# Optimization experiments

Measured on AMD Instinct MI355X. Metric: run time of the kernel, lower is better.

Reference implementation:

```python
import jax, jax.numpy as jnp
import numpy as np

N = 50000      # nodes
E = 800000     # edges (before self-loops)
NFEAT = 128
NHID = 32
H = 8
NCLASS = 47
NEG_SLOPE = 0.2  # PyG GATv2Conv default


def gatv2_layer(x, src, dst, Wl, Wr, att, b, n):
    """One GATv2Conv layer (concat over heads). att: [H, C]."""
    h, c = att.shape
    xl = (x @ Wl).reshape(n, h, c)  # source transform (lin_l)
    xr = (x @ Wr).reshape(n, h, c)  # target transform (lin_r)
    e = jax.nn.leaky_relu(xl[src] + xr[dst], NEG_SLOPE)   # [E, H, C]
    logits = jnp.einsum('ehc,hc->eh', e, att)             # [E, H]
    # segment softmax over incoming edges of each target node
    m = jax.ops.segment_max(logits, dst, num_segments=n)  # [N, H]
    alpha = jnp.exp(logits - m[dst])
    denom = jax.ops.segment_sum(alpha, dst, num_segments=n)
    alpha = alpha / (denom[dst] + 1e-16)
    msg = xl[src] * alpha[:, :, None]                     # [E, H, C]
    out = jax.ops.segment_sum(msg, dst, num_segments=n)   # [N, H, C]
    return out.reshape(n, h * c) + b


def setup_inputs():
    key = jax.random.key(0)
    ks = jax.random.split(key, 16)
    s = 0.1
    x = jax.random.normal(ks[0], (N, NFEAT), jnp.float32)
    edge_index = jax.random.randint(ks[1], (2, E), 0, N)
    HID = H * NHID  # 256
    params = dict(
        Wl0=jax.random.normal(ks[2], (NFEAT, HID), jnp.float32) * s,
        Wr0=jax.random.normal(ks[3], (NFEAT, HID), jnp.float32) * s,
        a0=jax.random.normal(ks[4], (H, NHID), jnp.float32) * s,
        b0=jnp.zeros((HID,), jnp.float32),
        Wl1=jax.random.normal(ks[5], (HID, HID), jnp.float32) * s,
        Wr1=jax.random.normal(ks[6], (HID, HID), jnp.float32) * s,
        a1=jax.random.normal(ks[7], (H, NHID), jnp.float32) * s,
        b1=jnp.zeros((HID,), jnp.float32),
        Wl2=jax.random.normal(ks[8], (HID, NCLASS), jnp.float32) * s,
        Wr2=jax.random.normal(ks[9], (HID, NCLASS), jnp.float32) * s,
        a2=jax.random.normal(ks[10], (1, NCLASS), jnp.float32) * s,
        b2=jnp.zeros((NCLASS,), jnp.float32),
    )
    return {"x": x, "edge_index": edge_index, **params}


def reference(x, edge_index, Wl0, Wr0, a0, b0, Wl1, Wr1, a1, b1, Wl2, Wr2, a2, b2):
    n = x.shape[0]
    # PyG GATv2Conv adds self-loops by default
    loops = jnp.arange(n, dtype=edge_index.dtype)
    src = jnp.concatenate([edge_index[0], loops])
    dst = jnp.concatenate([edge_index[1], loops])
    h = gatv2_layer(x, src, dst, Wl0, Wr0, a0, b0, n)
    h = jax.nn.elu(h)
    h = gatv2_layer(h, src, dst, Wl1, Wr1, a1, b1, n)
    h = jax.nn.elu(h)
    h = gatv2_layer(h, src, dst, Wl2, Wr2, a2, b2, n)
    return jax.nn.log_softmax(h, axis=-1)
```

## Files before the change

kernel.cpp:

```cpp
#include <hip/hip_runtime.h>
#include <cmath>


#define NFEAT 128
#define HID 256
#define NCLS 47
#define L2PAD 64
#define LOG2E 1.44269504088896340736f

typedef __attribute__((ext_vector_type(8))) short bf16x8;
typedef __attribute__((ext_vector_type(4))) float f32x4;
typedef __attribute__((ext_vector_type(2))) float f32x2;

__device__ __forceinline__ unsigned short f2b(float f) {
  unsigned int u = __builtin_bit_cast(unsigned int, f);
  u += 0x7FFFu + ((u >> 16) & 1u);
  return (unsigned short)(u >> 16);
}
__device__ __forceinline__ float b2f(unsigned short s) {
  return __builtin_bit_cast(float, (unsigned int)s << 16);
}
__device__ __forceinline__ f32x2 b2f2(unsigned int u) {
  return (f32x2){__builtin_bit_cast(float, u << 16),
                 __builtin_bit_cast(float, u & 0xFFFF0000u)};
}
__device__ __forceinline__ void glds16(const unsigned short* g, unsigned short* l) {
  __builtin_amdgcn_global_load_lds(
      (const __attribute__((address_space(1))) unsigned int*)g,
      (__attribute__((address_space(3))) unsigned int*)l, 16, 0, 0);
}

__global__ void k_cast_bf16(const float* __restrict__ in,
                            unsigned short* __restrict__ out, int n4,
                            int* __restrict__ deg, int n) {
  int i = blockIdx.x * blockDim.x + threadIdx.x;
  if (i < n4) {
    float4 v = reinterpret_cast<const float4*>(in)[i];
    ushort4 o = {f2b(v.x), f2b(v.y), f2b(v.z), f2b(v.w)};
    reinterpret_cast<ushort4*>(out)[i] = o;
  } else {
    int j = i - n4;
    if (j < n) deg[j] = 1;
  }
}

struct WtArgs {
  const float* W[6];
  unsigned short* WT[6];
  int K[6], M[6], off[6], total;
  const float* att;
  float* att48;
};
__global__ void k_wt_all(WtArgs a) {
  int i = blockIdx.x * blockDim.x + threadIdx.x;
  if (i >= a.total) {
    int j = i - a.total;
    if (j < 48) a.att48[j] = (j < NCLS) ? a.att[j] * LOG2E : 0.f;
    return;
  }
  int s = 0;
  #pragma unroll
  for (int j = 1; j < 6; ++j) if (i >= a.off[j]) s = j;
  int jj = i - a.off[s];
  int K = a.K[s], M = a.M[s];
  int m = jj / K, k = jj - m * K;
  a.WT[s][jj] = (m < M) ? f2b(a.W[s][(size_t)k * M + m]) : (unsigned short)0;
}

__global__ void k_count(const int* __restrict__ dst, int* __restrict__ deg, int e) {
  int i = blockIdx.x * blockDim.x + threadIdx.x;
  if (i < e) atomicAdd(&deg[dst[i]], 1);
}

__global__ __launch_bounds__(256) void k_bsum(const int* __restrict__ deg,
                                              int* __restrict__ bsum, int n) {
  int t = threadIdx.x;
  int base = blockIdx.x * 1024 + t * 4;
  int s = 0;
  if (base + 3 < n) {
    int4 v = *reinterpret_cast<const int4*>(deg + base);
    s = v.x + v.y + v.z + v.w;
  } else {
    for (int j = 0; j < 4; ++j) { int i = base + j; if (i < n) s += deg[i]; }
  }
  #pragma unroll
  for (int off = 1; off < 64; off <<= 1) s += __shfl_xor(s, off, 64);
  __shared__ int wsum[4];
  if ((t & 63) == 0) wsum[t >> 6] = s;
  __syncthreads();
  if (t == 0) bsum[blockIdx.x] = wsum[0] + wsum[1] + wsum[2] + wsum[3];
}

__global__ void k_scanb(int* __restrict__ bsum, int nb) {
  int lane = threadIdx.x;
  int v = (lane < nb) ? bsum[lane] : 0;
  #pragma unroll
  for (int off = 1; off < 64; off <<= 1) {
    int u = __shfl_up(v, off, 64);
    if (lane >= off) v += u;
  }
  if (lane < nb) bsum[lane] = v;
}

__global__ __launch_bounds__(256) void k_scanfinal(const int* __restrict__ deg,
                                                   const int* __restrict__ bscan,
                                                   int* __restrict__ rowptr,
                                                   int* __restrict__ adj,
                                                   int* __restrict__ vdst,
                                                   int* __restrict__ cursor, int n) {
  int t = threadIdx.x, b = blockIdx.x;
  int base = b * 1024 + t * 4;
  int v0 = 0, v1 = 0, v2 = 0, v3 = 0;
  if (base + 3 < n) {
    int4 v = *reinterpret_cast<const int4*>(deg + base);
    v0 = v.x; v1 = v.y; v2 = v.z; v3 = v.w;
  } else {
    if (base < n) v0 = deg[base];
    if (base + 1 < n) v1 = deg[base + 1];
    if (base + 2 < n) v2 = deg[base + 2];
    if (base + 3 < n) v3 = deg[base + 3];
  }
  int s = v0 + v1 + v2 + v3;
  int incl = s;
  #pragma unroll
  for (int off = 1; off < 64; off <<= 1) {
    int u = __shfl_up(incl, off, 64);
    if ((t & 63) >= off) incl += u;
  }
  __shared__ int wsum[4];
  int w = t >> 6, l = t & 63;
  if (l == 63) wsum[w] = incl;
  __syncthreads();
  int woff = 0;
  for (int j = 0; j < w; ++j) woff += wsum[j];
  int excl = incl - s + woff;
  int boff = (b == 0) ? 0 : bscan[b - 1];
  int p0 = boff + excl;
  int p1 = p0 + v0, p2 = p1 + v1, p3 = p2 + v2, p4 = p3 + v3;
  if (base < n)     { rowptr[base + 1] = p1; adj[p0] = base;     vdst[p0] = base;     cursor[base]     = p0 + 1; }
  if (base + 1 < n) { rowptr[base + 2] = p2; adj[p1] = base + 1; vdst[p1] = base + 1; cursor[base + 1] = p1 + 1; }
  if (base + 2 < n) { rowptr[base + 3] = p3; adj[p2] = base + 2; vdst[p2] = base + 2; cursor[base + 2] = p2 + 1; }
  if (base + 3 < n) { rowptr[base + 4] = p4; adj[p3] = base + 3; vdst[p3] = base + 3; cursor[base + 3] = p3 + 1; }
  if (b == 0 && t == 0) rowptr[0] = 0;
}

__global__ void k_scatter(const int* __restrict__ src, const int* __restrict__ dst,
                          int* __restrict__ cursor, int* __restrict__ adj,
                          int* __restrict__ vdst, int e) {
  int i = blockIdx.x * blockDim.x + threadIdx.x;
  if (i < e) {
    int d = dst[i];
    int p = atomicAdd(&cursor[d], 1);
    adj[p] = src[i];
    vdst[p] = d;
  }
}

__global__ __launch_bounds__(512) void gemm_dual_bf16_128(
    const unsigned short* __restrict__ X, const unsigned short* __restrict__ WlT,
    const unsigned short* __restrict__ WrT, unsigned short* __restrict__ XL,
    unsigned short* __restrict__ XR, int N, int K, int Mpad) {
  __shared__ __align__(16) unsigned short S[3 * 128 * 64];
  unsigned short* Xs = S;
  unsigned short* Ls = S + 8192;
  unsigned short* Rs = S + 16384;

  const int t = threadIdx.x;
  const int col0 = blockIdx.x * 128;
  const int row0 = blockIdx.y * 128;
  const int w = t >> 6, lane = t & 63;
  const int wr = w >> 2, wc = w & 3;
  const int r15 = lane & 15, kc = lane >> 4;
  const bool tail = (row0 + 128 > N);

  const int row_a = t >> 3,          c16_a = t & 7;
  const int row_b = (t + 512) >> 3,  c16_b = t & 7;
  const int sg_a = (c16_a ^ (row_a & 7)) * 8;
  const int sg_b = (c16_b ^ (row_b & 7)) * 8;
  unsigned short* d0 = S + w * 512;
  unsigned short* d1 = S + 4096 + w * 512;

  f32x4 accL[4][2], accR[4][2];
  #pragma unroll
  for (int rf = 0; rf < 4; ++rf)
    #pragma unroll
    for (int cf = 0; cf < 2; ++cf) {
      accL[rf][cf] = (f32x4){0.f, 0.f, 0.f, 0.f};
      accR[rf][cf] = (f32x4){0.f, 0.f, 0.f, 0.f};
    }

  for (int k0 = 0; k0 < K; k0 += 64) {
    glds16(WlT + (size_t)(col0 + row_a) * K + k0 + sg_a, d0 + 8192);
    glds16(WlT + (size_t)(col0 + row_b) * K + k0 + sg_b, d1 + 8192);
    glds16(WrT + (size_t)(col0 + row_a) * K + k0 + sg_a, d0 + 16384);
    glds16(WrT + (size_t)(col0 + row_b) * K + k0 + sg_b, d1 + 16384);
    if (!tail) {
      glds16(X + (size_t)(row0 + row_a) * K + k0 + sg_a, d0);
      glds16(X + (size_t)(row0 + row_b) * K + k0 + sg_b, d1);
    } else {
      uint4 va = (uint4){0, 0, 0, 0}, vb = (uint4){0, 0, 0, 0};
      if (row0 + row_a < N)
        va = *reinterpret_cast<const uint4*>(X + (size_t)(row0 + row_a) * K + k0 + sg_a);
      if (row0 + row_b < N)
        vb = *reinterpret_cast<const uint4*>(X + (size_t)(row0 + row_b) * K + k0 + sg_b);
      *reinterpret_cast<uint4*>(Xs + row_a * 64 + c16_a * 8) = va;
      *reinterpret_cast<uint4*>(Xs + row_b * 64 + c16_b * 8) = vb;
    }
    __syncthreads();

    #pragma unroll
    for (int ks = 0; ks < 2; ++ks) {
      const int c16 = ks * 4 + kc;
      bf16x8 a[4];
      #pragma unroll
      for (int rf = 0; rf < 4; ++rf) {
        const int rA = wr * 64 + rf * 16 + r15;
        a[rf] = *reinterpret_cast<const bf16x8*>(Xs + rA * 64 + ((c16 ^ (rA & 7)) * 8));
      }
      #pragma unroll
      for (int cf = 0; cf < 2; ++cf) {
        const int rB = wc * 32 + cf * 16 + r15;
        const int so = rB * 64 + ((c16 ^ (rB & 7)) * 8);
        const bf16x8 bl = *reinterpret_cast<const bf16x8*>(Ls + so);
        const bf16x8 br = *reinterpret_cast<const bf16x8*>(Rs + so);
        #pragma unroll
        for (int rf = 0; rf < 4; ++rf) {
          accL[rf][cf] = __builtin_amdgcn_mfma_f32_16x16x32_bf16(a[rf], bl, accL[rf][cf], 0, 0, 0);
          accR[rf][cf] = __builtin_amdgcn_mfma_f32_16x16x32_bf16(a[rf], br, accR[rf][cf], 0, 0, 0);
        }
      }
    }
    __syncthreads();
  }

  #pragma unroll
  for (int rf = 0; rf < 4; ++rf) {
    #pragma unroll
    for (int cf = 0; cf < 2; ++cf) {
      int cc = col0 + wc * 32 + cf * 16 + r15;
      #pragma unroll
      for (int i = 0; i < 4; ++i) {
        int rr = row0 + wr * 64 + rf * 16 + kc * 4 + i;
        if (rr < N) {
          XL[(size_t)rr * Mpad + cc] = f2b(accL[rf][cf][i]);
          XR[(size_t)rr * Mpad + cc] = f2b(accR[rf][cf][i]);
        }
      }
    }
  }
}

__global__ __launch_bounds__(256) void gemm_dual_bf16(
    const unsigned short* __restrict__ X, const unsigned short* __restrict__ WlT,
    const unsigned short* __restrict__ WrT, unsigned short* __restrict__ XL,
    unsigned short* __restrict__ XR, int N, int K, int Mpad) {
  __shared__ __align__(16) unsigned short S[3 * 64 * 64];
  unsigned short* Xs = S;
  unsigned short* Ls = S + 4096;
  unsigned short* Rs = S + 8192;

  const int t = threadIdx.x;
  const int col0 = blockIdx.x * 64;
  const int row0 = blockIdx.y * 64;
  const int w = t >> 6, lane = t & 63;
  const int r15 = lane & 15, kc = lane >> 4;
  const bool tail = (row0 + 64 > N);

  const int rowa = t >> 3, c16a = t & 7;
  const int rowb = (t + 256) >> 3, c16b = t & 7;
  const int sga = (c16a ^ (rowa & 7)) * 8;
  const int sgb = (c16b ^ (rowb & 7)) * 8;
  unsigned short* ldst0 = S + (w * 512);
  unsigned short* ldst1 = S + (2048 + w * 512);

  f32x4 accL[4], accR[4];
  #pragma unroll
  for (int i = 0; i < 4; ++i) {
    accL[i] = (f32x4){0.f, 0.f, 0.f, 0.f};
    accR[i] = (f32x4){0.f, 0.f, 0.f, 0.f};
  }

  const int rA = 16 * w + r15;

  for (int k0 = 0; k0 < K; k0 += 64) {
    glds16(WlT + (size_t)(col0 + rowa) * K + k0 + sga, ldst0 + 4096);
    glds16(WlT + (size_t)(col0 + rowb) * K + k0 + sgb, ldst1 + 4096);
    glds16(WrT + (size_t)(col0 + rowa) * K + k0 + sga, ldst0 + 8192);
    glds16(WrT + (size_t)(col0 + rowb) * K + k0 + sgb, ldst1 + 8192);
    if (!tail) {
      glds16(X + (size_t)(row0 + rowa) * K + k0 + sga, ldst0);
      glds16(X + (size_t)(row0 + rowb) * K + k0 + sgb, ldst1);
    } else {
      uint4 va = (uint4){0, 0, 0, 0}, vb = (uint4){0, 0, 0, 0};
      if (row0 + rowa < N)
        va = *reinterpret_cast<const uint4*>(X + (size_t)(row0 + rowa) * K + k0 + sga);
      if (row0 + rowb < N)
        vb = *reinterpret_cast<const uint4*>(X + (size_t)(row0 + rowb) * K + k0 + sgb);
      *reinterpret_cast<uint4*>(Xs + rowa * 64 + c16a * 8) = va;
      *reinterpret_cast<uint4*>(Xs + rowb * 64 + c16b * 8) = vb;
    }
    __syncthreads();

    #pragma unroll
    for (int ks = 0; ks < 2; ++ks) {
      const int c16 = ks * 4 + kc;
      const bf16x8 a = *reinterpret_cast<const bf16x8*>(
          Xs + rA * 64 + ((c16 ^ (rA & 7)) * 8));
      #pragma unroll
      for (int nf = 0; nf < 4; ++nf) {
        const int rB = nf * 16 + r15;
        const int so = rB * 64 + ((c16 ^ (rB & 7)) * 8);
        const bf16x8 bl = *reinterpret_cast<const bf16x8*>(Ls + so);
        const bf16x8 br = *reinterpret_cast<const bf16x8*>(Rs + so);
        accL[nf] = __builtin_amdgcn_mfma_f32_16x16x32_bf16(a, bl, accL[nf], 0, 0, 0);
        accR[nf] = __builtin_amdgcn_mfma_f32_16x16x32_bf16(a, br, accR[nf], 0, 0, 0);
      }
    }
    __syncthreads();
  }

  #pragma unroll
  for (int nf = 0; nf < 4; ++nf) {
    int cc = col0 + nf * 16 + r15;
    #pragma unroll
    for (int i = 0; i < 4; ++i) {
      int rr = row0 + 16 * w + kc * 4 + i;
      if (rr < N) {
        XL[(size_t)rr * Mpad + cc] = f2b(accL[nf][i]);
        XR[(size_t)rr * Mpad + cc] = f2b(accR[nf][i]);
      }
    }
  }
}

__global__ __launch_bounds__(1024) void gat_node_hc(
    const unsigned short* __restrict__ xl, const unsigned short* __restrict__ xr,
    const float* __restrict__ att, const float* __restrict__ bias,
    const int* __restrict__ rowptr, const int* __restrict__ adj,
    unsigned short* __restrict__ out, int n) {
  int wid = (blockIdx.x * blockDim.x + threadIdx.x) >> 6;
  int lane = threadIdx.x & 63;
  if (wid >= n) return;
  const int q = lane & 31, half = lane >> 5;

  const uint4 xrp = *reinterpret_cast<const uint4*>(xr + (size_t)wid * HID + q * 8);
  const f32x2 xr2[4] = {b2f2(xrp.x), b2f2(xrp.y), b2f2(xrp.z), b2f2(xrp.w)};
  const float4 af0 = *reinterpret_cast<const float4*>(att + q * 8);
  const float4 af1 = *reinterpret_cast<const float4*>(att + q * 8 + 4);
  const f32x2 a2[4] = {{af0.x, af0.y}, {af0.z, af0.w},
                       {af1.x, af1.y}, {af1.z, af1.w}};

  float m = -1e30f, denom = 0.f;
  f32x2 acc[4] = {{0.f, 0.f}, {0.f, 0.f}, {0.f, 0.f}, {0.f, 0.f}};

  const int beg = rowptr[wid], end = rowptr[wid + 1];
  int i = beg + half;
  bool act = i < end;
  int u = adj[act ? i : beg];
  uint4 p = *reinterpret_cast<const uint4*>(xl + (size_t)u * HID + q * 8);

  for (int base = beg; base < end; base += 2) {
    const int i2 = base + 2 + half;
    const bool act2 = i2 < end;
    const int u2 = adj[act2 ? i2 : beg];
    const uint4 p2 = *reinterpret_cast<const uint4*>(xl + (size_t)u2 * HID + q * 8);

    const f32x2 x2[4] = {b2f2(p.x), b2f2(p.y), b2f2(p.z), b2f2(p.w)};
    f32x2 s2 = {0.f, 0.f};
    #pragma unroll
    for (int j = 0; j < 4; ++j) {
      f32x2 z = x2[j] + xr2[j];
      f32x2 lz = 0.2f * z;
      f32x2 r = {fmaxf(z.x, lz.x), fmaxf(z.y, lz.y)};
      s2 += r * a2[j];
    }
    float part = s2.x + s2.y;
    part += __shfl_xor(part, 1, 64);
    part += __shfl_xor(part, 2, 64);
    if (!act) part = -1e30f;
    if (__any(part > m + 8.f)) {
      float mn = fmaxf(m, part);
      float so = __expf(m - mn);
      float wn = act ? __expf(part - mn) : 0.f;
      denom = denom * so + wn;
      #pragma unroll
      for (int j = 0; j < 4; ++j) acc[j] = acc[j] * so + wn * x2[j];
      m = mn;
    } else {
      float wn = act ? __expf(part - m) : 0.f;
      denom += wn;
      #pragma unroll
      for (int j = 0; j < 4; ++j) acc[j] += wn * x2[j];
    }
    p = p2;
    act = act2;
  }

  float mo = __shfl_xor(m, 32, 64);
  float ms = fmaxf(m, mo);
  float sc = __expf(m - ms);
  denom *= sc;
  denom += __shfl_xor(denom, 32, 64);
  #pragma unroll
  for (int j = 0; j < 4; ++j) {
    acc[j] *= sc;
    acc[j].x += __shfl_xor(acc[j].x, 32, 64);
    acc[j].y += __shfl_xor(acc[j].y, 32, 64);
  }

  if (half == 0) {
    const float inv = 1.f / (denom + 1e-16f);
    const float4 bf0 = *reinterpret_cast<const float4*>(bias + q * 8);
    const float4 bf1 = *reinterpret_cast<const float4*>(bias + q * 8 + 4);
    float o[8] = {acc[0].x * inv + bf0.x, acc[0].y * inv + bf0.y,
                  acc[1].x * inv + bf0.z, acc[1].y * inv + bf0.w,
                  acc[2].x * inv + bf1.x, acc[2].y * inv + bf1.y,
                  acc[3].x * inv + bf1.z, acc[3].y * inv + bf1.w};
    #pragma unroll
    for (int j = 0; j < 8; ++j) o[j] = o[j] > 0.f ? o[j] : (__expf(o[j]) - 1.f);
    uint4 ov;
    ov.x = (unsigned)f2b(o[0]) | ((unsigned)f2b(o[1]) << 16);
    ov.y = (unsigned)f2b(o[2]) | ((unsigned)f2b(o[3]) << 16);
    ov.z = (unsigned)f2b(o[4]) | ((unsigned)f2b(o[5]) << 16);
    ov.w = (unsigned)f2b(o[6]) | ((unsigned)f2b(o[7]) << 16);
    *reinterpret_cast<uint4*>(out + (size_t)wid * HID + q * 8) = ov;
  }
}

__global__ __launch_bounds__(256) void k_logit_l2(
    const unsigned short* __restrict__ xl, const unsigned short* __restrict__ xr,
    const float* __restrict__ att48, const int* __restrict__ adj,
    const int* __restrict__ vdst, float* __restrict__ logit, int total) {
  int i = blockIdx.x * blockDim.x + threadIdx.x;
  if (i >= total) return;
  const int u = adj[i], v = vdst[i];
  const uint4* pu = reinterpret_cast<const uint4*>(xl + (size_t)u * L2PAD);
  const uint4* pv = reinterpret_cast<const uint4*>(xr + (size_t)v * L2PAD);
  f32x2 s2 = {0.f, 0.f};
  #pragma unroll
  for (int b = 0; b < 6; ++b) {
    const uint4 xu = pu[b], xv = pv[b];
    const f32x2* a2 = reinterpret_cast<const f32x2*>(att48 + b * 8);
    const unsigned ua[4] = {xu.x, xu.y, xu.z, xu.w};
    const unsigned va[4] = {xv.x, xv.y, xv.z, xv.w};
    #pragma unroll
    for (int j = 0; j < 4; ++j) {
      f32x2 z = b2f2(ua[j]) + b2f2(va[j]);
      f32x2 lz = 0.2f * z;
      f32x2 r = {fmaxf(z.x, lz.x), fmaxf(z.y, lz.y)};
      s2 += r * a2[j];
    }
  }
  logit[i] = s2.x + s2.y;
}

__global__ __launch_bounds__(1024) void gat_node_l2(
    const unsigned short* __restrict__ xl, const float* __restrict__ logit,
    const float* __restrict__ bias, const int* __restrict__ rowptr,
    const int* __restrict__ adj, float* __restrict__ out, int n) {
  int wid = (blockIdx.x * blockDim.x + threadIdx.x) >> 6;
  int lane = threadIdx.x & 63;
  if (wid >= n) return;
  const bool act = lane < NCLS;
  const int beg = rowptr[wid], end = rowptr[wid + 1];

  float mx = -1e30f;
  for (int i = beg + lane; i < end; i += 64) mx = fmaxf(mx, logit[i]);
  #pragma unroll
  for (int off = 1; off < 64; off <<= 1) mx = fmaxf(mx, __shfl_xor(mx, off, 64));

  float denom = 0.f, acc = 0.f;
  int i = beg;
  for (; i + 1 < end; i += 2) {
    int u0 = adj[i], u1 = adj[i + 1];
    float w0 = exp2f(logit[i] - mx);
    float w1 = exp2f(logit[i + 1] - mx);
    float x0 = act ? b2f(xl[(size_t)u0 * L2PAD + lane]) : 0.f;
    float x1 = act ? b2f(xl[(size_t)u1 * L2PAD + lane]) : 0.f;
    denom += w0 + w1;
    acc += w0 * x0 + w1 * x1;
  }
  if (i < end) {
    int u0 = adj[i];
    float w0 = exp2f(logit[i] - mx);
    float x0 = act ? b2f(xl[(size_t)u0 * L2PAD + lane]) : 0.f;
    denom += w0;
    acc += w0 * x0;
  }

  float r = acc / (denom + 1e-16f) + (act ? bias[lane] : 0.f);
  float rm = act ? r : -1e30f;
  #pragma unroll
  for (int off = 1; off < 64; off <<= 1) rm = fmaxf(rm, __shfl_xor(rm, off, 64));
  float se = act ? __expf(r - rm) : 0.f;
  #pragma unroll
  for (int off = 1; off < 64; off <<= 1) se += __shfl_xor(se, off, 64);
  if (act) out[(size_t)wid * NCLS + lane] = r - rm - __logf(se);
}

extern "C" void kernel_launch(void* const* d_in, const int* in_sizes, int n_in,
                              void* d_out, int out_size, void* d_ws, size_t ws_size,
                              hipStream_t stream) {
  const float* x   = (const float*)d_in[0];
  const int* ei    = (const int*)d_in[1];
  const float* Wl0 = (const float*)d_in[2];
  const float* Wr0 = (const float*)d_in[3];
  const float* a0  = (const float*)d_in[4];
  const float* b0  = (const float*)d_in[5];
  const float* Wl1 = (const float*)d_in[6];
  const float* Wr1 = (const float*)d_in[7];
  const float* a1  = (const float*)d_in[8];
  const float* b1  = (const float*)d_in[9];
  const float* Wl2 = (const float*)d_in[10];
  const float* Wr2 = (const float*)d_in[11];
  const float* a2  = (const float*)d_in[12];
  const float* b2  = (const float*)d_in[13];

  const int N = in_sizes[0] / NFEAT;
  const int E = in_sizes[1] / 2;
  const int* src = ei;
  const int* dst = ei + E;
  const int total = E + N;

  char* ws = (char*)d_ws;
  unsigned short* xlb = (unsigned short*)ws; ws += (size_t)N * HID * 2;
  unsigned short* xrb = (unsigned short*)ws; ws += (size_t)N * HID * 2;
  unsigned short* xb  = (unsigned short*)ws; ws += (size_t)N * HID * 2;
  unsigned short* hb  = (unsigned short*)ws; ws += (size_t)N * HID * 2;
  unsigned short* WT  = (unsigned short*)ws; ws += (size_t)6 * HID * HID * 2;
  float* logit = (float*)ws; ws += (size_t)total * sizeof(float);
  float* att48 = (float*)ws; ws += 64 * sizeof(float);
  int* deg    = (int*)ws; ws += (size_t)N * sizeof(int);
  int* rowptr = (int*)ws; ws += (size_t)(N + 8) * sizeof(int);
  int* bsum   = (int*)ws; ws += (size_t)64 * sizeof(int);
  int* adj    = (int*)ws; ws += (size_t)total * sizeof(int);
  int* vdst   = (int*)ws; ws += (size_t)total * sizeof(int);

  unsigned short* WlT0 = WT + 0 * HID * HID;
  unsigned short* WrT0 = WT + 1 * HID * HID;
  unsigned short* WlT1 = WT + 2 * HID * HID;
  unsigned short* WrT1 = WT + 3 * HID * HID;
  unsigned short* WlT2 = WT + 4 * HID * HID;
  unsigned short* WrT2 = WT + 5 * HID * HID;

  const int TB = 256;
  const int nbScan = (N + 1023) / 1024;
  const int n4 = N * NFEAT / 4;

  k_cast_bf16<<<(n4 + N + TB - 1) / TB, TB, 0, stream>>>(x, xb, n4, deg, N);
  {
    WtArgs a;
    const float* Wsrc[6] = {Wl0, Wr0, Wl1, Wr1, Wl2, Wr2};
    unsigned short* Wdst[6] = {WlT0, WrT0, WlT1, WrT1, WlT2, WrT2};
    int Ks[6] = {NFEAT, NFEAT, HID, HID, HID, HID};
    int Ms[6] = {HID, HID, HID, HID, NCLS, NCLS};
    int Mp[6] = {HID, HID, HID, HID, L2PAD, L2PAD};
    int off = 0;
    for (int s = 0; s < 6; ++s) {
      a.W[s] = Wsrc[s]; a.WT[s] = Wdst[s]; a.K[s] = Ks[s]; a.M[s] = Ms[s];
      a.off[s] = off; off += Mp[s] * Ks[s];
    }
    a.total = off;
    a.att = a2; a.att48 = att48;
    k_wt_all<<<(a.total + 48 + TB - 1) / TB, TB, 0, stream>>>(a);
  }

  k_count<<<(E + TB - 1) / TB, TB, 0, stream>>>(dst, deg, E);
  k_bsum<<<nbScan, TB, 0, stream>>>(deg, bsum, N);
  k_scanb<<<1, 64, 0, stream>>>(bsum, nbScan);
  k_scanfinal<<<nbScan, TB, 0, stream>>>(deg, bsum, rowptr, adj, vdst, deg, N);
  k_scatter<<<(E + TB - 1) / TB, TB, 0, stream>>>(src, dst, deg, adj, vdst, E);

  const int nodeBlocks = (N + 15) / 16;
  const int rb128 = (N + 127) / 128;
  const int rb64 = (N + 63) / 64;

  {
    dim3 g(HID / 128, rb128);
    gemm_dual_bf16_128<<<g, 512, 0, stream>>>(xb, WlT0, WrT0, xlb, xrb, N, NFEAT, HID);
    gat_node_hc<<<nodeBlocks, 1024, 0, stream>>>(xlb, xrb, a0, b0, rowptr, adj, hb, N);
  }
  {
    dim3 g(HID / 128, rb128);
    gemm_dual_bf16_128<<<g, 512, 0, stream>>>(hb, WlT1, WrT1, xlb, xrb, N, HID, HID);
    gat_node_hc<<<nodeBlocks, 1024, 0, stream>>>(xlb, xrb, a1, b1, rowptr, adj, xb, N);
  }
  {
    dim3 g(1, rb64);
    gemm_dual_bf16<<<g, 256, 0, stream>>>(xb, WlT2, WrT2, xlb, xrb, N, HID, L2PAD);
    k_logit_l2<<<(total + TB - 1) / TB, TB, 0, stream>>>(xlb, xrb, att48, adj,
                                                         vdst, logit, total);
    gat_node_l2<<<nodeBlocks, 1024, 0, stream>>>(xlb, logit, b2, rowptr, adj,
                                                 (float*)d_out, N);
  }
}
```

Before: 448.7 us.

## Interleave CSR src/dst, use DPP quad sum, shrink node blocks, unroll l2 gather

Merges the separate adj and vdst arrays into one int2 CSR array, so the scatter and logit kernels do a single 8-byte access per edge. In gat_node_hc it drops the software prefetch of the next neighbour row and replaces the shuffle-based 4-lane reduction with DPP moves. Node kernels go from 1024-thread to 256-thread blocks, and the layer-2 aggregation loop is unrolled by four to put more gathers in flight. Removing the prefetch may expose gather latency, and the interleaved layout doubles the bytes read when only src is needed.

```diff
diff --git a/kernel.cpp b/kernel.cpp
--- a/kernel.cpp
+++ b/kernel.cpp
@@ -28,6 +28,14 @@
   __builtin_amdgcn_global_load_lds(
       (const __attribute__((address_space(1))) unsigned int*)g,
       (__attribute__((address_space(3))) unsigned int*)l, 16, 0, 0);
+}
+
+__device__ __forceinline__ float quad_sum(float v) {
+  int t = __builtin_amdgcn_mov_dpp(__builtin_bit_cast(int, v), 0xB1, 0xF, 0xF, true);
+  v += __builtin_bit_cast(float, t);
+  t = __builtin_amdgcn_mov_dpp(__builtin_bit_cast(int, v), 0x4E, 0xF, 0xF, true);
+  v += __builtin_bit_cast(float, t);
+  return v;
 }
 
 __global__ void k_cast_bf16(const float* __restrict__ in,
@@ -105,8 +113,7 @@
 __global__ __launch_bounds__(256) void k_scanfinal(const int* __restrict__ deg,
                                                    const int* __restrict__ bscan,
                                                    int* __restrict__ rowptr,
-                                                   int* __restrict__ adj,
-                                                   int* __restrict__ vdst,
+                                                   int2* __restrict__ csr,
                                                    int* __restrict__ cursor, int n) {
   int t = threadIdx.x, b = blockIdx.x;
   int base = b * 1024 + t * 4;
@@ -137,22 +144,20 @@
   int boff = (b == 0) ? 0 : bscan[b - 1];
   int p0 = boff + excl;
   int p1 = p0 + v0, p2 = p1 + v1, p3 = p2 + v2, p4 = p3 + v3;
-  if (base < n)     { rowptr[base + 1] = p1; adj[p0] = base;     vdst[p0] = base;     cursor[base]     = p0 + 1; }
-  if (base + 1 < n) { rowptr[base + 2] = p2; adj[p1] = base + 1; vdst[p1] = base + 1; cursor[base + 1] = p1 + 1; }
-  if (base + 2 < n) { rowptr[base + 3] = p3; adj[p2] = base + 2; vdst[p2] = base + 2; cursor[base + 2] = p2 + 1; }
-  if (base + 3 < n) { rowptr[base + 4] = p4; adj[p3] = base + 3; vdst[p3] = base + 3; cursor[base + 3] = p3 + 1; }
+  if (base < n)     { rowptr[base + 1] = p1; csr[p0] = make_int2(base, base);         cursor[base]     = p0 + 1; }
+  if (base + 1 < n) { rowptr[base + 2] = p2; csr[p1] = make_int2(base + 1, base + 1); cursor[base + 1] = p1 + 1; }
+  if (base + 2 < n) { rowptr[base + 3] = p3; csr[p2] = make_int2(base + 2, base + 2); cursor[base + 2] = p2 + 1; }
+  if (base + 3 < n) { rowptr[base + 4] = p4; csr[p3] = make_int2(base + 3, base + 3); cursor[base + 3] = p3 + 1; }
   if (b == 0 && t == 0) rowptr[0] = 0;
 }
 
 __global__ void k_scatter(const int* __restrict__ src, const int* __restrict__ dst,
-                          int* __restrict__ cursor, int* __restrict__ adj,
-                          int* __restrict__ vdst, int e) {
+                          int* __restrict__ cursor, int2* __restrict__ csr, int e) {
   int i = blockIdx.x * blockDim.x + threadIdx.x;
   if (i < e) {
     int d = dst[i];
     int p = atomicAdd(&cursor[d], 1);
-    adj[p] = src[i];
-    vdst[p] = d;
+    csr[p] = make_int2(src[i], d);
   }
 }
 
@@ -333,10 +338,10 @@
   }
 }
 
-__global__ __launch_bounds__(1024) void gat_node_hc(
+__global__ __launch_bounds__(256) void gat_node_hc(
     const unsigned short* __restrict__ xl, const unsigned short* __restrict__ xr,
     const float* __restrict__ att, const float* __restrict__ bias,
-    const int* __restrict__ rowptr, const int* __restrict__ adj,
+    const int* __restrict__ rowptr, const int2* __restrict__ csr,
     unsigned short* __restrict__ out, int n) {
   int wid = (blockIdx.x * blockDim.x + threadIdx.x) >> 6;
   int lane = threadIdx.x & 63;
@@ -354,17 +359,12 @@
   f32x2 acc[4] = {{0.f, 0.f}, {0.f, 0.f}, {0.f, 0.f}, {0.f, 0.f}};
 
   const int beg = rowptr[wid], end = rowptr[wid + 1];
-  int i = beg + half;
-  bool act = i < end;
-  int u = adj[act ? i : beg];
-  uint4 p = *reinterpret_cast<const uint4*>(xl + (size_t)u * HID + q * 8);
-
+  const int* csr_src = reinterpret_cast<const int*>(csr);
   for (int base = beg; base < end; base += 2) {
-    const int i2 = base + 2 + half;
-    const bool act2 = i2 < end;
-    const int u2 = adj[act2 ? i2 : beg];
-    const uint4 p2 = *reinterpret_cast<const uint4*>(xl + (size_t)u2 * HID + q * 8);
-
+    const int i = base + half;
+    const bool act = i < end;
+    const int u = csr_src[2 * (act ? i : base)];
+    const uint4 p = *reinterpret_cast<const uint4*>(xl + (size_t)u * HID + q * 8);
     const f32x2 x2[4] = {b2f2(p.x), b2f2(p.y), b2f2(p.z), b2f2(p.w)};
     f32x2 s2 = {0.f, 0.f};
     #pragma unroll
@@ -374,9 +374,7 @@
       f32x2 r = {fmaxf(z.x, lz.x), fmaxf(z.y, lz.y)};
       s2 += r * a2[j];
     }
-    float part = s2.x + s2.y;
-    part += __shfl_xor(part, 1, 64);
-    part += __shfl_xor(part, 2, 64);
+    float part = quad_sum(s2.x + s2.y);
     if (!act) part = -1e30f;
     if (__any(part > m + 8.f)) {
       float mn = fmaxf(m, part);
@@ -392,8 +390,6 @@
       #pragma unroll
       for (int j = 0; j < 4; ++j) acc[j] += wn * x2[j];
     }
-    p = p2;
-    act = act2;
   }
 
   float mo = __shfl_xor(m, 32, 64);
@@ -429,13 +425,13 @@
 
 __global__ __launch_bounds__(256) void k_logit_l2(
     const unsigned short* __restrict__ xl, const unsigned short* __restrict__ xr,
-    const float* __restrict__ att48, const int* __restrict__ adj,
-    const int* __restrict__ vdst, float* __restrict__ logit, int total) {
+    const float* __restrict__ att48, const int2* __restrict__ csr,
+    float* __restrict__ logit, int total) {
   int i = blockIdx.x * blockDim.x + threadIdx.x;
   if (i >= total) return;
-  const int u = adj[i], v = vdst[i];
-  const uint4* pu = reinterpret_cast<const uint4*>(xl + (size_t)u * L2PAD);
-  const uint4* pv = reinterpret_cast<const uint4*>(xr + (size_t)v * L2PAD);
+  const int2 e = csr[i];
+  const uint4* pu = reinterpret_cast<const uint4*>(xl + (size_t)e.x * L2PAD);
+  const uint4* pv = reinterpret_cast<const uint4*>(xr + (size_t)e.y * L2PAD);
   f32x2 s2 = {0.f, 0.f};
   #pragma unroll
   for (int b = 0; b < 6; ++b) {
@@ -454,15 +450,16 @@
   logit[i] = s2.x + s2.y;
 }
 
-__global__ __launch_bounds__(1024) void gat_node_l2(
+__global__ __launch_bounds__(256) void gat_node_l2(
     const unsigned short* __restrict__ xl, const float* __restrict__ logit,
     const float* __restrict__ bias, const int* __restrict__ rowptr,
-    const int* __restrict__ adj, float* __restrict__ out, int n) {
+    const int2* __restrict__ csr, float* __restrict__ out, int n) {
   int wid = (blockIdx.x * blockDim.x + threadIdx.x) >> 6;
   int lane = threadIdx.x & 63;
   if (wid >= n) return;
   const bool act = lane < NCLS;
   const int beg = rowptr[wid], end = rowptr[wid + 1];
+  const int* csr_src = reinterpret_cast<const int*>(csr);
 
   float mx = -1e30f;
   for (int i = beg + lane; i < end; i += 64) mx = fmaxf(mx, logit[i]);
@@ -470,22 +467,22 @@
   for (int off = 1; off < 64; off <<= 1) mx = fmaxf(mx, __shfl_xor(mx, off, 64));
 
   float denom = 0.f, acc = 0.f;
-  int i = beg;
-  for (; i + 1 < end; i += 2) {
-    int u0 = adj[i], u1 = adj[i + 1];
-    float w0 = exp2f(logit[i] - mx);
-    float w1 = exp2f(logit[i + 1] - mx);
-    float x0 = act ? b2f(xl[(size_t)u0 * L2PAD + lane]) : 0.f;
-    float x1 = act ? b2f(xl[(size_t)u1 * L2PAD + lane]) : 0.f;
-    denom += w0 + w1;
-    acc += w0 * x0 + w1 * x1;
-  }
-  if (i < end) {
-    int u0 = adj[i];
-    float w0 = exp2f(logit[i] - mx);
-    float x0 = act ? b2f(xl[(size_t)u0 * L2PAD + lane]) : 0.f;
-    denom += w0;
-    acc += w0 * x0;
+  for (int base = beg; base < end; base += 4) {
+    int i1 = base + 1, i2 = base + 2, i3 = base + 3;
+    const bool a1 = i1 < end, a2v = i2 < end, a3 = i3 < end;
+    i1 = a1 ? i1 : base; i2 = a2v ? i2 : base; i3 = a3 ? i3 : base;
+    const int u0 = csr_src[2 * base], u1 = csr_src[2 * i1];
+    const int u2 = csr_src[2 * i2],  u3 = csr_src[2 * i3];
+    const float x0 = act ? b2f(xl[(size_t)u0 * L2PAD + lane]) : 0.f;
+    const float x1 = act ? b2f(xl[(size_t)u1 * L2PAD + lane]) : 0.f;
+    const float x2 = act ? b2f(xl[(size_t)u2 * L2PAD + lane]) : 0.f;
+    const float x3 = act ? b2f(xl[(size_t)u3 * L2PAD + lane]) : 0.f;
+    float w0 = exp2f(logit[base] - mx);
+    float w1 = a1 ? exp2f(logit[i1] - mx) : 0.f;
+    float w2 = a2v ? exp2f(logit[i2] - mx) : 0.f;
+    float w3 = a3 ? exp2f(logit[i3] - mx) : 0.f;
+    denom += (w0 + w1) + (w2 + w3);
+    acc += (w0 * x0 + w1 * x1) + (w2 * x2 + w3 * x3);
   }
 
   float r = acc / (denom + 1e-16f) + (act ? bias[lane] : 0.f);
@@ -533,8 +530,7 @@
   int* deg    = (int*)ws; ws += (size_t)N * sizeof(int);
   int* rowptr = (int*)ws; ws += (size_t)(N + 8) * sizeof(int);
   int* bsum   = (int*)ws; ws += (size_t)64 * sizeof(int);
-  int* adj    = (int*)ws; ws += (size_t)total * sizeof(int);
-  int* vdst   = (int*)ws; ws += (size_t)total * sizeof(int);
+  int2* csr   = (int2*)ws; ws += (size_t)total * sizeof(int2);
 
   unsigned short* WlT0 = WT + 0 * HID * HID;
   unsigned short* WrT0 = WT + 1 * HID * HID;
@@ -568,29 +564,29 @@
   k_count<<<(E + TB - 1) / TB, TB, 0, stream>>>(dst, deg, E);
   k_bsum<<<nbScan, TB, 0, stream>>>(deg, bsum, N);
   k_scanb<<<1, 64, 0, stream>>>(bsum, nbScan);
-  k_scanfinal<<<nbScan, TB, 0, stream>>>(deg, bsum, rowptr, adj, vdst, deg, N);
-  k_scatter<<<(E + TB - 1) / TB, TB, 0, stream>>>(src, dst, deg, adj, vdst, E);
-
-  const int nodeBlocks = (N + 15) / 16;
+  k_scanfinal<<<nbScan, TB, 0, stream>>>(deg, bsum, rowptr, csr, deg, N);
+  k_scatter<<<(E + TB - 1) / TB, TB, 0, stream>>>(src, dst, deg, csr, E);
+
+  const int nodeBlocks = (N + 3) / 4;
   const int rb128 = (N + 127) / 128;
   const int rb64 = (N + 63) / 64;
 
   {
     dim3 g(HID / 128, rb128);
     gemm_dual_bf16_128<<<g, 512, 0, stream>>>(xb, WlT0, WrT0, xlb, xrb, N, NFEAT, HID);
-    gat_node_hc<<<nodeBlocks, 1024, 0, stream>>>(xlb, xrb, a0, b0, rowptr, adj, hb, N);
+    gat_node_hc<<<nodeBlocks, 256, 0, stream>>>(xlb, xrb, a0, b0, rowptr, csr, hb, N);
   }
   {
     dim3 g(HID / 128, rb128);
     gemm_dual_bf16_128<<<g, 512, 0, stream>>>(hb, WlT1, WrT1, xlb, xrb, N, HID, HID);
-    gat_node_hc<<<nodeBlocks, 1024, 0, stream>>>(xlb, xrb, a1, b1, rowptr, adj, xb, N);
+    gat_node_hc<<<nodeBlocks, 256, 0, stream>>>(xlb, xrb, a1, b1, rowptr, csr, xb, N);
   }
   {
     dim3 g(1, rb64);
     gemm_dual_bf16<<<g, 256, 0, stream>>>(xb, WlT2, WrT2, xlb, xrb, N, HID, L2PAD);
-    k_logit_l2<<<(total + TB - 1) / TB, TB, 0, stream>>>(xlb, xrb, att48, adj,
-                                                         vdst, logit, total);
-    gat_node_l2<<<nodeBlocks, 1024, 0, stream>>>(xlb, logit, b2, rowptr, adj,
-                                                 (float*)d_out, N);
-  }
-}
+    k_logit_l2<<<(total + TB - 1) / TB, TB, 0, stream>>>(xlb, xrb, att48, csr,
+                                                         logit, total);
+    gat_node_l2<<<nodeBlocks, 256, 0, stream>>>(xlb, logit, b2, rowptr, csr,
+                                                (float*)d_out, N);
+  }
+}
```

After: 432.5 us. 1.04x faster.
